# Kernel tuning notes

Hardware: AMD Instinct MI355X
Metric: run time of the kernel (lower is better)

Reference implementation:

```python
import jax, jax.numpy as jnp
import numpy as np

# dims: batch, parity, l-dims of in1/in2, output l-dim, channels
B, P, L1, L2, N, F = 8192, 2, 9, 9, 25, 128

MASK_EVEN = jnp.array([[1.0], [0.0]], dtype=jnp.float32)  # [2,1]
MASK_ODD = jnp.array([[0.0], [1.0]], dtype=jnp.float32)   # [2,1]


def setup_inputs() -> dict:
    key = jax.random.key(0)
    k1, k2, k3 = jax.random.split(key, 3)
    x1 = jax.random.normal(k1, (B, P, L1, F), dtype=jnp.float32)
    x2 = jax.random.normal(k2, (B, P, L2, F), dtype=jnp.float32)
    # Clebsch-Gordan tensor is an nn.Parameter in the module; random init is
    # equivalent for correctness testing of the contraction math.
    cg = jax.random.normal(k3, (L1, L2, N), dtype=jnp.float32)
    return {"x1": x1, "x2": x2, "cg": cg}


def reference(x1, x2, cg):
    # pseudotensor path of TensorProduct.forward with channel_dim='f'
    def couple(m1, m2):
        a = jnp.einsum('bplf,pa->balf', x1, m1)  # parity mask projection, a=1
        b = jnp.einsum('bplf,pa->balf', x2, m2)
        # triple contraction against CG tensor: [B,1,N,F]
        return jnp.einsum('balf,bamf,lmn->banf', a, b, cg)

    # NOTE: original code calls _couple_slices('even','odd') for BOTH eee and
    # eoo — reproduced faithfully.
    eee = couple(MASK_EVEN, MASK_ODD)
    ooe = couple(MASK_ODD, MASK_EVEN)
    eoo = couple(MASK_EVEN, MASK_ODD)
    oeo = couple(MASK_ODD, MASK_ODD)
    # stack along axis=-3 -> [B, 1, 2, N, F]
    return jnp.stack((eee + ooe, eoo + oeo), axis=-3)
```

## Files before the change

### kernel.cpp

```cpp
#include <hip/hip_runtime.h>


#define B_DIM 8192
#define F_DIM 128
#define L_DIM 9
#define N_DIM 25

typedef __attribute__((ext_vector_type(2))) float v2f;

__global__ __launch_bounds__(256) void tp_kernel(
    const float* __restrict__ x1,
    const float* __restrict__ x2,
    const float* __restrict__ cg,
    float* __restrict__ out)
{
    const int g = blockIdx.x * 256 + threadIdx.x;
    const int b = g >> 7;
    const int f = g & 127;

    const float* x1b = x1 + (size_t)b * 2 * L_DIM * F_DIM + f;
    const float* x2b = x2 + (size_t)b * 2 * L_DIM * F_DIM + f;

    v2f x2p[L_DIM];
#pragma unroll
    for (int m = 0; m < L_DIM; ++m) {
        v2f v;
        v.x = __builtin_nontemporal_load(&x2b[m * F_DIM]);
        v.y = __builtin_nontemporal_load(&x2b[(L_DIM + m) * F_DIM]);
        x2p[m] = v;
    }

    v2f acc[N_DIM];
#pragma unroll
    for (int n = 0; n < N_DIM; ++n) { acc[n] = (v2f)(0.0f); }

#pragma unroll 1
    for (int l = 0; l < L_DIM; ++l) {
        const float x1e = __builtin_nontemporal_load(&x1b[l * F_DIM]);
        const float x1o = __builtin_nontemporal_load(&x1b[(L_DIM + l) * F_DIM]);
        v2f x1o2; x1o2.x = x1o; x1o2.y = x1o;
        const float* cp_l = cg + l * (L_DIM * N_DIM);
#pragma unroll
        for (int m = 0; m < L_DIM; ++m) {
            const float t = x1e * x2p[m].y;
            v2f tt; tt.x = t; tt.y = t;
            const v2f s = __builtin_elementwise_fma(x1o2, x2p[m], tt);
#pragma unroll
            for (int n = 0; n < N_DIM; ++n) {
                const float c = cp_l[m * N_DIM + n];
                v2f cc; cc.x = c; cc.y = c;
                acc[n] = __builtin_elementwise_fma(cc, s, acc[n]);
            }
        }
    }

    float* ob = out + (size_t)b * 2 * N_DIM * F_DIM + f;
#pragma unroll
    for (int n = 0; n < N_DIM; ++n) {
        __builtin_nontemporal_store(acc[n].x, &ob[n * F_DIM]);
        __builtin_nontemporal_store(acc[n].y, &ob[(N_DIM + n) * F_DIM]);
    }
}

extern "C" void kernel_launch(void* const* d_in, const int* in_sizes, int n_in,
                              void* d_out, int out_size, void* d_ws, size_t ws_size,
                              hipStream_t stream) {
    (void)in_sizes; (void)n_in; (void)out_size; (void)d_ws; (void)ws_size;
    const float* x1 = (const float*)d_in[0];
    const float* x2 = (const float*)d_in[1];
    const float* cg = (const float*)d_in[2];
    float* out = (float*)d_out;

    const int threads = 256;
    const int blocks  = (B_DIM * F_DIM) / threads;
    tp_kernel<<<blocks, threads, 0, stream>>>(x1, x2, cg, out);
}
```

Baseline: 344.8 us.

## Compute CG contraction with FP16 MFMA via shared-memory staged outer products

Replaces the per-thread FP32 FMA loop over l,m,n with a two-stage scheme. Each block first forms the 81 parity-combined outer products per channel in FP16 and stages them in LDS. It then contracts them against the CG tensor using 16x16x32 f16 MFMA instructions, with the CG matrix pre-packed into fragment layout by a small prep kernel. This moves the compute-heavy contraction onto matrix cores at the cost of FP16 rounding of both operands, which may hurt accuracy, plus an extra kernel launch and LDS traffic.

```diff
diff --git a/kernel.cpp b/kernel.cpp
--- a/kernel.cpp
+++ b/kernel.cpp
@@ -1,65 +1,172 @@
 #include <hip/hip_runtime.h>
+#include <stdint.h>
 
 
 #define B_DIM 8192
 #define F_DIM 128
 #define L_DIM 9
 #define N_DIM 25
+#define K_DIM 81
+#define ROW_U32 52
+#define CH_U32 (F_DIM * ROW_U32)
 
-typedef __attribute__((ext_vector_type(2))) float v2f;
+typedef _Float16 half8 __attribute__((ext_vector_type(8)));
+typedef _Float16 half2v __attribute__((ext_vector_type(2)));
+typedef float f32x4 __attribute__((ext_vector_type(4)));
 
-__global__ __launch_bounds__(256) void tp_kernel(
+__device__ __align__(16) uint4 g_fragA[2 * 3 * 64];
+
+__global__ __launch_bounds__(256) void cg_prep(const float* __restrict__ cg) {
+    for (int e = threadIdx.x; e < 2 * 3 * 64; e += 256) {
+        const int fid  = e >> 6;
+        const int lane = e & 63;
+        const int mtile = fid / 3, kstep = fid - 3 * mtile;
+        const int n     = mtile * 16 + (lane & 15);
+        const int kbase = kstep * 32 + (lane >> 4) * 8;
+        uint32_t w[4];
+        for (int j = 0; j < 4; ++j) {
+            const int k0 = kbase + 2 * j, k1 = k0 + 1;
+            const float v0 = (k0 < K_DIM && n < N_DIM) ? cg[k0 * N_DIM + n] : 0.0f;
+            const float v1 = (k1 < K_DIM && n < N_DIM) ? cg[k1 * N_DIM + n] : 0.0f;
+            w[j] = __builtin_bit_cast(uint32_t, __builtin_amdgcn_cvt_pkrtz(v0, v1));
+        }
+        g_fragA[e] = make_uint4(w[0], w[1], w[2], w[3]);
+    }
+}
+
+__global__ __launch_bounds__(256, 3) void tp_kernel(
     const float* __restrict__ x1,
     const float* __restrict__ x2,
-    const float* __restrict__ cg,
     float* __restrict__ out)
 {
-    const int g = blockIdx.x * 256 + threadIdx.x;
-    const int b = g >> 7;
-    const int f = g & 127;
+    __shared__ uint32_t S[2 * CH_U32];
+    const int b = blockIdx.x;
+    const int t = threadIdx.x;
+    const int lane = t & 63;
 
-    const float* x1b = x1 + (size_t)b * 2 * L_DIM * F_DIM + f;
-    const float* x2b = x2 + (size_t)b * 2 * L_DIM * F_DIM + f;
+    uint4 afr[2][3];
+#pragma unroll
+    for (int mt = 0; mt < 2; ++mt)
+#pragma unroll
+        for (int ks = 0; ks < 3; ++ks)
+            afr[mt][ks] = g_fragA[(mt * 3 + ks) * 64 + lane];
 
-    v2f x2p[L_DIM];
+    const int f     = t & 127;
+    const int khalf = t >> 7;
+
+    const float* x1b = x1 + (size_t)b * (2 * L_DIM * F_DIM) + f;
+    const float* x2b = x2 + (size_t)b * (2 * L_DIM * F_DIM) + f;
+
+    float x2e[L_DIM], x2o[L_DIM];
 #pragma unroll
     for (int m = 0; m < L_DIM; ++m) {
-        v2f v;
-        v.x = __builtin_nontemporal_load(&x2b[m * F_DIM]);
-        v.y = __builtin_nontemporal_load(&x2b[(L_DIM + m) * F_DIM]);
-        x2p[m] = v;
+        x2e[m] = x2b[m * F_DIM];
+        x2o[m] = x2b[(L_DIM + m) * F_DIM];
     }
 
-    v2f acc[N_DIM];
+    uint32_t* Srow0 = S + f * ROW_U32 + khalf * 24;
+    uint32_t* Srow1 = Srow0 + CH_U32;
+
+    if (khalf == 0) {
+        float x1e[6], x1o[6];
 #pragma unroll
-    for (int n = 0; n < N_DIM; ++n) { acc[n] = (v2f)(0.0f); }
+        for (int l = 0; l < 6; ++l) {
+            x1e[l] = x1b[l * F_DIM];
+            x1o[l] = x1b[(L_DIM + l) * F_DIM];
+        }
+#pragma unroll
+        for (int j = 0; j < 12; ++j) {
+            float s0[4], s1[4];
+#pragma unroll
+            for (int kk = 0; kk < 4; ++kk) {
+                const int k = 4 * j + kk;
+                const int l = k / 9, m = k % 9;
+                const float tt = x1e[l] * x2o[m];
+                s0[kk] = fmaf(x1o[l], x2e[m], tt);
+                s1[kk] = fmaf(x1o[l], x2o[m], tt);
+            }
+            uint2 w0, w1;
+            w0.x = __builtin_bit_cast(uint32_t, __builtin_amdgcn_cvt_pkrtz(s0[0], s0[1]));
+            w0.y = __builtin_bit_cast(uint32_t, __builtin_amdgcn_cvt_pkrtz(s0[2], s0[3]));
+            w1.x = __builtin_bit_cast(uint32_t, __builtin_amdgcn_cvt_pkrtz(s1[0], s1[1]));
+            w1.y = __builtin_bit_cast(uint32_t, __builtin_amdgcn_cvt_pkrtz(s1[2], s1[3]));
+            *reinterpret_cast<uint2*>(Srow0 + 2 * j) = w0;
+            *reinterpret_cast<uint2*>(Srow1 + 2 * j) = w1;
+        }
+    } else {
+        float x1e[4], x1o[4];
+#pragma unroll
+        for (int l = 0; l < 4; ++l) {
+            x1e[l] = x1b[(5 + l) * F_DIM];
+            x1o[l] = x1b[(L_DIM + 5 + l) * F_DIM];
+        }
+#pragma unroll
+        for (int j = 0; j < 12; ++j) {
+            float s0[4], s1[4];
+#pragma unroll
+            for (int kk = 0; kk < 4; ++kk) {
+                const int k = 48 + 4 * j + kk;
+                if (k < K_DIM) {
+                    const int l = k / 9 - 5, m = k % 9;
+                    const float tt = x1e[l] * x2o[m];
+                    s0[kk] = fmaf(x1o[l], x2e[m], tt);
+                    s1[kk] = fmaf(x1o[l], x2o[m], tt);
+                } else { s0[kk] = 0.0f; s1[kk] = 0.0f; }
+            }
+            uint2 w0, w1;
+            w0.x = __builtin_bit_cast(uint32_t, __builtin_amdgcn_cvt_pkrtz(s0[0], s0[1]));
+            w0.y = __builtin_bit_cast(uint32_t, __builtin_amdgcn_cvt_pkrtz(s0[2], s0[3]));
+            w1.x = __builtin_bit_cast(uint32_t, __builtin_amdgcn_cvt_pkrtz(s1[0], s1[1]));
+            w1.y = __builtin_bit_cast(uint32_t, __builtin_amdgcn_cvt_pkrtz(s1[2], s1[3]));
+            *reinterpret_cast<uint2*>(Srow0 + 2 * j) = w0;
+            *reinterpret_cast<uint2*>(Srow1 + 2 * j) = w1;
+        }
+    }
+    __syncthreads();
 
-#pragma unroll 1
-    for (int l = 0; l < L_DIM; ++l) {
-        const float x1e = __builtin_nontemporal_load(&x1b[l * F_DIM]);
-        const float x1o = __builtin_nontemporal_load(&x1b[(L_DIM + l) * F_DIM]);
-        v2f x1o2; x1o2.x = x1o; x1o2.y = x1o;
-        const float* cp_l = cg + l * (L_DIM * N_DIM);
+    const int wv = t >> 6;
+    const int ch = wv & 1;
+    const int fq = wv >> 1;
+    const int r  = lane & 15, g4 = lane >> 4;
+
+    f32x4 acc[2][4];
 #pragma unroll
-        for (int m = 0; m < L_DIM; ++m) {
-            const float t = x1e * x2p[m].y;
-            v2f tt; tt.x = t; tt.y = t;
-            const v2f s = __builtin_elementwise_fma(x1o2, x2p[m], tt);
+    for (int mt = 0; mt < 2; ++mt)
 #pragma unroll
-            for (int n = 0; n < N_DIM; ++n) {
-                const float c = cp_l[m * N_DIM + n];
-                v2f cc; cc.x = c; cc.y = c;
-                acc[n] = __builtin_elementwise_fma(cc, s, acc[n]);
+        for (int nt = 0; nt < 4; ++nt)
+            acc[mt][nt] = (f32x4)(0.0f);
+
+    const uint32_t* Sch = S + ch * CH_U32;
+#pragma unroll
+    for (int nt = 0; nt < 4; ++nt) {
+        const int ntile = fq * 4 + nt;
+        const uint32_t* base = Sch + (ntile * 16 + r) * ROW_U32 + g4 * 4;
+#pragma unroll
+        for (int ks = 0; ks < 3; ++ks) {
+            const uint4 bw = *reinterpret_cast<const uint4*>(base + ks * 16);
+            const half8 bh = __builtin_bit_cast(half8, bw);
+#pragma unroll
+            for (int mt = 0; mt < 2; ++mt) {
+                const half8 ah = __builtin_bit_cast(half8, afr[mt][ks]);
+                acc[mt][nt] = __builtin_amdgcn_mfma_f32_16x16x32_f16(
+                    ah, bh, acc[mt][nt], 0, 0, 0);
             }
         }
     }
 
-    float* ob = out + (size_t)b * 2 * N_DIM * F_DIM + f;
+    float* ob = out + (size_t)b * (2 * N_DIM * F_DIM) + (size_t)ch * (N_DIM * F_DIM);
 #pragma unroll
-    for (int n = 0; n < N_DIM; ++n) {
-        __builtin_nontemporal_store(acc[n].x, &ob[n * F_DIM]);
-        __builtin_nontemporal_store(acc[n].y, &ob[(N_DIM + n) * F_DIM]);
-    }
+    for (int mt = 0; mt < 2; ++mt)
+#pragma unroll
+        for (int nt = 0; nt < 4; ++nt) {
+            const int fcol = (fq * 4 + nt) * 16 + r;
+#pragma unroll
+            for (int j = 0; j < 4; ++j) {
+                const int n = mt * 16 + g4 * 4 + j;
+                if (n < N_DIM)
+                    __builtin_nontemporal_store(acc[mt][nt][j], ob + n * F_DIM + fcol);
+            }
+        }
 }
 
 extern "C" void kernel_launch(void* const* d_in, const int* in_sizes, int n_in,
@@ -71,7 +178,7 @@
     const float* cg = (const float*)d_in[2];
     float* out = (float*)d_out;
 
-    const int threads = 256;
-    const int blocks  = (B_DIM * F_DIM) / threads;
-    tp_kernel<<<blocks, threads, 0, stream>>>(x1, x2, cg, out);
+    cg_prep<<<1, 256, 0, stream>>>(cg);
+
+    tp_kernel<<<B_DIM, 256, 0, stream>>>(x1, x2, out);
 }
```

New measurement: 323.3 us. -6.2%, faster.
